# Performance work log

Measured on AMD Instinct MI355X. Metric: run time of the kernel, lower is better.

Reference implementation:

```python
import jax, jax.numpy as jnp
import numpy as np

B, S, F_IN, H, F_OUT, BB = 128, 1024, 128, 256, 128, 256


def setup_inputs() -> dict:
    key = jax.random.key(0)
    ks = jax.random.split(key, 16)
    s_in = 1.0 / np.sqrt(F_IN + H)
    s_bb = 1.0 / np.sqrt(BB)
    s_h = 1.0 / np.sqrt(H)
    return {
        "x": jax.random.normal(ks[0], (B, S, F_IN), dtype=jnp.float32),
        "ts": jax.random.uniform(ks[1], (B, S), dtype=jnp.float32),
        # backbone (depth=1): Linear(F_IN+H -> BB)
        "Wb": jax.random.normal(ks[2], (F_IN + H, BB), dtype=jnp.float32) * s_in,
        "bb": jnp.zeros((BB,), jnp.float32),
        # CfC heads: ff1, ff2, time_a, time_b (BB -> H)
        "Wff1": jax.random.normal(ks[3], (BB, H), dtype=jnp.float32) * s_bb,
        "bff1": jnp.zeros((H,), jnp.float32),
        "Wff2": jax.random.normal(ks[4], (BB, H), dtype=jnp.float32) * s_bb,
        "bff2": jnp.zeros((H,), jnp.float32),
        "Wta": jax.random.normal(ks[5], (BB, H), dtype=jnp.float32) * s_bb,
        "bta": jnp.zeros((H,), jnp.float32),
        "Wtb": jax.random.normal(ks[6], (BB, H), dtype=jnp.float32) * s_bb,
        "btb": jnp.zeros((H,), jnp.float32),
        # output projection Linear(H -> F_OUT)
        "Wout": jax.random.normal(ks[7], (H, F_OUT), dtype=jnp.float32) * s_h,
        "bout": jnp.zeros((F_OUT,), jnp.float32),
    }


def reference(x, ts, Wb, bb, Wff1, bff1, Wff2, bff2, Wta, bta, Wtb, btb, Wout, bout):
    # x: [B,S,F_IN], ts: [B,S] -> out: [B,S,F_OUT]
    batch = x.shape[0]
    hidden = Wff1.shape[1]

    def step(h, inp):
        xt, tt = inp  # xt: [B,F_IN], tt: [B]
        z = jnp.tanh(jnp.concatenate([xt, h], axis=-1) @ Wb + bb)  # backbone [B,BB]
        ff1 = jnp.tanh(z @ Wff1 + bff1)
        ff2 = jnp.tanh(z @ Wff2 + bff2)
        t_a = z @ Wta + bta
        t_b = z @ Wtb + btb
        t_interp = jax.nn.sigmoid(t_a * tt[:, None] + t_b)  # time-dependent gate
        h_new = ff1 * (1.0 - t_interp) + t_interp * ff2
        y = h_new @ Wout + bout
        return h_new, y

    h0 = jnp.zeros((batch, hidden), dtype=x.dtype)
    xs = (jnp.swapaxes(x, 0, 1), jnp.swapaxes(ts, 0, 1))  # time-major for scan
    _, ys = jax.lax.scan(step, h0, xs)  # ys: [S,B,F_OUT]
    return jnp.swapaxes(ys, 0, 1)
```

## Files before the change

kernel.cpp:

```cpp
#include <hip/hip_runtime.h>

#define Bn   128
#define Sn   1024
#define FIN  128
#define Hn   256
#define FOUT 128
#define KBB  384
#define NT1  512

#define NR4 20
#define NL4 1
#define DYN_SMEM ((32 * 256 * 8 + NL4 * 1024 * 8) * 2)

#define WB_OFF 0
#define W4_OFF 98304
#define WO_OFF 360448
#define WS_HALVES 393216
#define HBUF_OFF WS_HALVES
#define XC_OFF (HBUF_OFF + (size_t)Bn * Sn * Hn)
#define WS_SPLIT_BYTES ((size_t)(WS_HALVES + (size_t)Bn * Sn * Hn) * 2)
#define WS_FULL_BYTES ((XC_OFF + (size_t)Bn * Sn * Hn) * 2)

typedef _Float16 h2 __attribute__((ext_vector_type(2)));
typedef _Float16 h8 __attribute__((ext_vector_type(8)));

__device__ __forceinline__ float dot2f(h2 a, h2 b, float c) {
#if __has_builtin(__builtin_amdgcn_fdot2)
  return __builtin_amdgcn_fdot2(a, b, c, false);
#else
  return c + (float)a[0] * (float)b[0] + (float)a[1] * (float)b[1];
#endif
}
__device__ __forceinline__ void dot8_4(h8 v, h8 w, float& c0, float& c1, float& c2, float& c3) {
  h2 v0 = {v[0], v[1]}, v1 = {v[2], v[3]}, v2 = {v[4], v[5]}, v3 = {v[6], v[7]};
  h2 w0 = {w[0], w[1]}, w1 = {w[2], w[3]}, w2 = {w[4], w[5]}, w3 = {w[6], w[7]};
  c0 = dot2f(v0, w0, c0); c1 = dot2f(v1, w1, c1);
  c2 = dot2f(v2, w2, c2); c3 = dot2f(v3, w3, c3);
}

__global__ __launch_bounds__(256) void pack_w(
    const float* __restrict__ Wb, const float* __restrict__ W1,
    const float* __restrict__ W2, const float* __restrict__ W3,
    const float* __restrict__ W4, const float* __restrict__ Wo,
    _Float16* __restrict__ ws) {
  int p = blockIdx.x * 256 + threadIdx.x;
  if (p >= WS_HALVES) return;
  float v;
  if (p < W4_OFF) {
    int r = p & 7, j = (p >> 3) & 255;
    int k = ((p >> 11) << 3) | r;
    v = Wb[k * 256 + j];
  } else if (p < WO_OFF) {
    int q = p - W4_OFF;
    int r = q & 7, j = (q >> 3) & 1023;
    int k = ((q >> 13) << 3) | r;
    int jj = j & 255;
    const float* Ws = (j < 256) ? W1 : (j < 512) ? W2 : (j < 768) ? W3 : W4;
    v = Ws[k * 256 + jj];
  } else {
    int q = p - WO_OFF;
    int r = q & 7, j = (q >> 3) & 127;
    int k = ((q >> 10) << 3) | r;
    v = Wo[k * 128 + j];
  }
  ws[p] = (_Float16)v;
}

__global__ __launch_bounds__(256) void xgemm(
    const float* __restrict__ x, const _Float16* __restrict__ ws,
    _Float16* __restrict__ xc) {
  __shared__ __align__(16) _Float16 sX[64 * 128];
  const int tid = threadIdx.x;
  const size_t r0 = (size_t)blockIdx.x * 64;
  const float* xb = x + r0 * 128;
#pragma unroll
  for (int m = 0; m < 32; ++m)
    sX[m * 256 + tid] = (_Float16)xb[m * 256 + tid];
  const _Float16* gX = ws + WB_OFF + (size_t)tid * 8;
  h8 wx[16];
#pragma unroll
  for (int L = 0; L < 16; ++L) wx[L] = *(const h8*)(gX + (size_t)L * 2048);
  __syncthreads();
  for (int r = 0; r < 64; ++r) {
    float c0 = 0.f, c1 = 0.f, c2 = 0.f, c3 = 0.f;
#pragma unroll
    for (int L = 0; L < 16; ++L) {
      h8 v = *(const h8*)&sX[r * 128 + L * 8];
      dot8_4(v, wx[L], c0, c1, c2, c3);
    }
    xc[(r0 + r) * 256 + tid] = (_Float16)(c0 + c1 + c2 + c3);
  }
}

template <int XC, int INLINE_Y>
__global__ __launch_bounds__(NT1, 2) void cfc5(
    const float* __restrict__ x, const float* __restrict__ ts,
    const float* __restrict__ bb, const float* __restrict__ bf1,
    const float* __restrict__ bf2, const float* __restrict__ bta,
    const float* __restrict__ btb, const float* __restrict__ bo,
    _Float16* __restrict__ ws, float* __restrict__ out) {
  __shared__ __align__(16) _Float16 xh[KBB];
  __shared__ __align__(16) _Float16 zf[Hn];
  __shared__ float tsb[Sn];
  __shared__ float scrZ[256];
  __shared__ float scrH[512];
  extern __shared__ __align__(16) _Float16 dyn[];
  _Float16* sWb  = dyn;
  _Float16* sW4L = dyn + 32 * 256 * 8;

  const int tid = threadIdx.x;
  const int b = blockIdx.x;
  const _Float16* Wb_p = ws + WB_OFF;
  const _Float16* W4_p = ws + W4_OFF;
  const _Float16* Wo_p = ws + WO_OFF;
  _Float16* hbuf = ws + HBUF_OFF;
  const _Float16* xcp = ws + XC_OFF;

  const float* xrow  = x  + (size_t)b * Sn * FIN;
  const float* tsrow = ts + (size_t)b * Sn;
  float*       orow  = out + (size_t)b * Sn * FOUT;

  const int jz = tid & 255, kz = tid >> 8;
  const float bbj = (tid < 256) ? bb[tid] : 0.f;
  const float bHA = (tid < 256) ? bf1[tid] : bf2[tid - 256];
  const float bHB = (tid < 256) ? bta[tid] : btb[tid - 256];
  const int jY = tid & 127, kqY = tid >> 7;
  const float boj = bo[jY];

  if (XC) {
    const h8* src = (const h8*)(Wb_p + (size_t)16 * 2048);
    h8* dst = (h8*)sWb;
    for (int i = tid; i < 8192; i += NT1) dst[i] = src[i];
  }
  {
    const h8* src = (const h8*)(W4_p + (size_t)NR4 * 8192);
    h8* dst = (h8*)sW4L;
    for (int i = tid; i < NL4 * 1024; i += NT1) dst[i] = src[i];
  }
  for (int i = tid; i < Sn; i += NT1) tsb[i] = tsrow[i];
  if (tid < 128) ((unsigned*)xh)[64 + tid] = 0;
  if (!XC && tid < 64) {
    float2 xv = *(const float2*)(xrow + 2 * tid);
    h2 p; p[0] = (_Float16)xv.x; p[1] = (_Float16)xv.y;
    *(h2*)&xh[2 * tid] = p;
  }

  const _Float16* gA = W4_p + (size_t)tid * 8;
  const _Float16* gB = W4_p + (size_t)(tid + 512) * 8;
  h8 wA[NR4], wBv[NR4];
#pragma unroll
  for (int c = 0; c < NR4; ++c) {
    wA[c]  = *(const h8*)(gA + (size_t)c * 8192);
    wBv[c] = *(const h8*)(gB + (size_t)c * 8192);
  }
#pragma unroll
  for (int c = 0; c < NR4; ++c) {
    asm volatile("" : "+v"(wA[c]));
    asm volatile("" : "+v"(wBv[c]));
  }
  __syncthreads();

  for (int st = 0; st < Sn; ++st) {
    float xcv = 0.f;
    if (XC && tid < 256)
      xcv = (float)xcp[((size_t)b * Sn + st) * 256 + tid];
    float2 xv; xv.x = 0.f; xv.y = 0.f;
    if (!XC && tid >= 448 && st + 1 < Sn)
      xv = *(const float2*)(xrow + (size_t)(st + 1) * FIN + 2 * (tid - 448));

    float a0 = 0.f, a1 = 0.f, a2 = 0.f, a3 = 0.f;
    if (XC) {
#pragma unroll 4
      for (int c = 0; c < 16; ++c) {
        int kc = kz * 16 + c;
        h8 v = *(const h8*)&xh[128 + kc * 8];
        h8 w = *(const h8*)&sWb[((size_t)kc * 256 + jz) * 8];
        dot8_4(v, w, a0, a1, a2, a3);
      }
    } else {
      const _Float16* gZ = Wb_p + ((size_t)(kz * 24) * 256 + jz) * 8;
#pragma unroll 4
      for (int c = 0; c < 24; ++c) {
        h8 v = *(const h8*)&xh[(kz * 24 + c) * 8];
        h8 w = *(const h8*)(gZ + (size_t)c * 2048);
        dot8_4(v, w, a0, a1, a2, a3);
      }
    }
    float zs = a0 + a1 + a2 + a3;
    if (kz) scrZ[jz] = zs;
    __syncthreads();
    if (tid < 256) {
      float zp = zs + scrZ[tid] + bbj;
      if (XC) zp += xcv;
      zf[tid] = (_Float16)tanhf(zp);
    }
    if (!XC && tid >= 448 && st + 1 < Sn) {
      h2 p; p[0] = (_Float16)xv.x; p[1] = (_Float16)xv.y;
      *(h2*)&xh[2 * (tid - 448)] = p;
    }
    __syncthreads();

    float hA0 = 0.f, hA1 = 0.f, hA2 = 0.f, hA3 = 0.f;
    float hB0 = 0.f, hB1 = 0.f, hB2 = 0.f, hB3 = 0.f;
#pragma unroll 2
    for (int c = NR4 + NL4; c < 32; ++c) {
      h8 v  = *(const h8*)&zf[c * 8];
      h8 wa = *(const h8*)(gA + (size_t)c * 8192);
      h8 wb = *(const h8*)(gB + (size_t)c * 8192);
      dot8_4(v, wa, hA0, hA1, hA2, hA3);
      dot8_4(v, wb, hB0, hB1, hB2, hB3);
    }
#pragma unroll
    for (int c = 0; c < NR4; ++c) {
      h8 v = *(const h8*)&zf[c * 8];
      dot8_4(v, wA[c],  hA0, hA1, hA2, hA3);
      dot8_4(v, wBv[c], hB0, hB1, hB2, hB3);
    }
#pragma unroll
    for (int l = 0; l < NL4; ++l) {
      h8 v  = *(const h8*)&zf[(NR4 + l) * 8];
      h8 wa = *(const h8*)&sW4L[((size_t)l * 1024 + tid) * 8];
      h8 wb = *(const h8*)&sW4L[((size_t)l * 1024 + tid + 512) * 8];
      dot8_4(v, wa, hA0, hA1, hA2, hA3);
      dot8_4(v, wb, hB0, hB1, hB2, hB3);
    }
    float gAv = hA0 + hA1 + hA2 + hA3 + bHA;
    float gBv = hB0 + hB1 + hB2 + hB3 + bHB;
    if (tid >= 256) {
      scrH[tid - 256]       = gAv;
      scrH[256 + tid - 256] = gBv;
    }
    __syncthreads();
    if (tid < 256) {
      float ff2v = scrH[tid], tbv = scrH[256 + tid];
      float tt = tsb[st];
      float sg = 1.f / (1.f + __expf(-(gBv * tt + tbv)));
      float hn = tanhf(gAv) * (1.f - sg) + sg * tanhf(ff2v);
      xh[128 + tid] = (_Float16)hn;
      if (!INLINE_Y)
        hbuf[((size_t)b * Sn + st) * Hn + tid] = (_Float16)hn;
    }
    __syncthreads();

    if (INLINE_Y) {
      const _Float16* gY = Wo_p + ((size_t)(kqY * 8) * 128 + jY) * 8;
      float y0 = 0.f, y1 = 0.f, y2 = 0.f, y3 = 0.f;
#pragma unroll
      for (int c = 0; c < 8; ++c) {
        h8 v = *(const h8*)&xh[128 + (kqY * 8 + c) * 8];
        h8 w = *(const h8*)(gY + (size_t)c * 1024);
        dot8_4(v, w, y0, y1, y2, y3);
      }
      float ysv = y0 + y1 + y2 + y3;
      if (kqY) scrH[(kqY - 1) * 128 + jY] = ysv;
      __syncthreads();
      if (kqY == 0) {
        float y = ysv + boj + scrH[jY] + scrH[128 + jY] + scrH[256 + jY];
        orow[(size_t)st * FOUT + jY] = y;
      }
    }
  }
}

#define SMEMY (65536 + 4096)
extern "C" __global__ __launch_bounds__(256, 4)
void ygemm(const _Float16* __restrict__ ws, const float* __restrict__ bo,
           float* __restrict__ out) {
  extern __shared__ char ysm[];
  _Float16* sWo = (_Float16*)ysm;
  _Float16* sH  = (_Float16*)(ysm + 65536);
  const int tid = threadIdx.x;
  { const uint4* g = (const uint4*)(ws + WO_OFF);
    uint4* l = (uint4*)sWo;
#pragma unroll
    for (int i = 0; i < 16; ++i) l[tid + 256 * i] = g[tid + 256 * i]; }
  const _Float16* hb = ws + HBUF_OFF;
  const int row0 = blockIdx.x * 256;
  const int j = tid & 127, rh = tid >> 7;
  const float boj = bo[j];
  for (int it = 0; it < 32; ++it) {
    const int rbase = row0 + it * 8;
    __syncthreads();
    ((uint4*)sH)[tid] = ((const uint4*)(hb + (size_t)rbase * 256))[tid];
    __syncthreads();
#pragma unroll
    for (int rr = rh; rr < 8; rr += 2) {
      float y0 = 0.f, y1 = 0.f, y2 = 0.f, y3 = 0.f;
#pragma unroll 4
      for (int c = 0; c < 32; ++c) {
        h8 v = *(const h8*)&sH[rr * 256 + c * 8];
        h8 w = *(const h8*)&sWo[((size_t)c * 128 + j) * 8];
        dot8_4(v, w, y0, y1, y2, y3);
      }
      out[(size_t)(rbase + rr) * 128 + j] = y0 + y1 + y2 + y3 + boj;
    }
  }
}

extern "C" void kernel_launch(void* const* d_in, const int* in_sizes, int n_in,
                              void* d_out, int out_size, void* d_ws, size_t ws_size,
                              hipStream_t stream) {
  const float* x   = (const float*)d_in[0];
  const float* ts  = (const float*)d_in[1];
  const float* Wb  = (const float*)d_in[2];
  const float* bb  = (const float*)d_in[3];
  const float* W1  = (const float*)d_in[4];
  const float* bf1 = (const float*)d_in[5];
  const float* W2  = (const float*)d_in[6];
  const float* bf2 = (const float*)d_in[7];
  const float* W3  = (const float*)d_in[8];
  const float* bta = (const float*)d_in[9];
  const float* W4  = (const float*)d_in[10];
  const float* btb = (const float*)d_in[11];
  const float* Wo  = (const float*)d_in[12];
  const float* bo  = (const float*)d_in[13];
  float* out = (float*)d_out;
  _Float16* ws = (_Float16*)d_ws;

  pack_w<<<WS_HALVES / 256, 256, 0, stream>>>(Wb, W1, W2, W3, W4, Wo, ws);

  if (ws_size >= WS_FULL_BYTES) {
    xgemm<<<(Bn * Sn) / 64, 256, 0, stream>>>(x, ws, ws + XC_OFF);
    hipFuncSetAttribute((const void*)(cfc5<1, 0>),
                        hipFuncAttributeMaxDynamicSharedMemorySize, DYN_SMEM);
    cfc5<1, 0><<<Bn, NT1, DYN_SMEM, stream>>>(x, ts, bb, bf1, bf2, bta, btb, bo, ws, out);
    hipFuncSetAttribute((const void*)ygemm,
                        hipFuncAttributeMaxDynamicSharedMemorySize, SMEMY);
    ygemm<<<(Bn * Sn) / 256, 256, SMEMY, stream>>>(ws, bo, out);
  } else if (ws_size >= WS_SPLIT_BYTES) {
    hipFuncSetAttribute((const void*)(cfc5<0, 0>),
                        hipFuncAttributeMaxDynamicSharedMemorySize, DYN_SMEM);
    cfc5<0, 0><<<Bn, NT1, DYN_SMEM, stream>>>(x, ts, bb, bf1, bf2, bta, btb, bo, ws, out);
    hipFuncSetAttribute((const void*)ygemm,
                        hipFuncAttributeMaxDynamicSharedMemorySize, SMEMY);
    ygemm<<<(Bn * Sn) / 256, 256, SMEMY, stream>>>(ws, bo, out);
  } else {
    hipFuncSetAttribute((const void*)(cfc5<0, 1>),
                        hipFuncAttributeMaxDynamicSharedMemorySize, DYN_SMEM);
    cfc5<0, 1><<<Bn, NT1, DYN_SMEM, stream>>>(x, ts, bb, bf1, bf2, bta, btb, bo, ws, out);
  }
}
```

Before: 4.162 ms.

## Split each recurrent batch row across two blocks with global mailbox exchange

Adds a kernel, cfc6, that assigns each batch row to two workgroups, each owning half of the hidden units, so the launch covers 256 blocks instead of 128. At every timestep each block computes a partial backbone pre-activation from its own half of h and posts it to a double-buffered global mailbox. It then bumps a per-block counter and spin-waits on the partner's counter before adding the partner's partial. The aim is to halve the per-block weight work in the serial time loop and keep more of each block's head weights resident in LDS and registers. The cost is a global-memory handshake on every step, and the scheme relies on both blocks of a pair being co-resident, or it can deadlock.

```diff
diff --git a/kernel.cpp b/kernel.cpp
--- a/kernel.cpp
+++ b/kernel.cpp
@@ -11,6 +11,10 @@
 #define NR4 20
 #define NL4 1
 #define DYN_SMEM ((32 * 256 * 8 + NL4 * 1024 * 8) * 2)
+
+#define NL6 11
+#define PF6 10
+#define DYN6 ((16 * 256 * 8 + NL6 * 512 * 8) * 2)
 
 #define WB_OFF 0
 #define W4_OFF 98304
@@ -20,6 +24,10 @@
 #define XC_OFF (HBUF_OFF + (size_t)Bn * Sn * Hn)
 #define WS_SPLIT_BYTES ((size_t)(WS_HALVES + (size_t)Bn * Sn * Hn) * 2)
 #define WS_FULL_BYTES ((XC_OFF + (size_t)Bn * Sn * Hn) * 2)
+#define MBOX_BYTE_OFF WS_FULL_BYTES
+#define MBOX_FLOATS ((size_t)Bn * 2 * 2 * 256)
+#define CNT_BYTE_OFF (MBOX_BYTE_OFF + MBOX_FLOATS * 4)
+#define WS_PAIR_BYTES (CNT_BYTE_OFF + 256 * 4)
 
 typedef _Float16 h2 __attribute__((ext_vector_type(2)));
 typedef _Float16 h8 __attribute__((ext_vector_type(8)));
@@ -66,6 +74,8 @@
   ws[p] = (_Float16)v;
 }
 
+__global__ void zcnt(unsigned* __restrict__ c) { c[threadIdx.x] = 0; }
+
 __global__ __launch_bounds__(256) void xgemm(
     const float* __restrict__ x, const _Float16* __restrict__ ws,
     _Float16* __restrict__ xc) {
@@ -89,6 +99,128 @@
       dot8_4(v, wx[L], c0, c1, c2, c3);
     }
     xc[(r0 + r) * 256 + tid] = (_Float16)(c0 + c1 + c2 + c3);
+  }
+}
+
+__global__ __launch_bounds__(NT1) void cfc6(
+    const float* __restrict__ ts, const float* __restrict__ bb,
+    const float* __restrict__ bf1, const float* __restrict__ bf2,
+    const float* __restrict__ bta, const float* __restrict__ btb,
+    _Float16* __restrict__ ws, unsigned* __restrict__ cnt,
+    float* __restrict__ mbox) {
+  __shared__ __align__(16) _Float16 hl[128];
+  __shared__ __align__(16) _Float16 zfs[Hn];
+  __shared__ float tsb[Sn];
+  __shared__ float scrZ[256];
+  __shared__ float scrH[384];
+  extern __shared__ __align__(16) _Float16 dyn[];
+  _Float16* sWbh = dyn;
+  _Float16* sW4L = dyn + 16 * 256 * 8;
+
+  const int tid = threadIdx.x;
+  const int row = blockIdx.x & 127;
+  const int hf  = blockIdx.x >> 7;
+
+  const _Float16* Wb_p = ws + WB_OFF;
+  const _Float16* W4_p = ws + W4_OFF;
+  _Float16* hbuf = ws + HBUF_OFF;
+  const _Float16* xcp = ws + XC_OFF;
+  const float* tsrow = ts + (size_t)row * Sn;
+
+  const int jz = tid & 255, kq = tid >> 8;
+  const int head = tid >> 7, jj = tid & 127;
+  const int jcol = head * 256 + hf * 128 + jj;
+  const float bbj = (tid < 256) ? bb[tid] : 0.f;
+  const float bH =
+      (head == 0 ? bf1 : head == 1 ? bf2 : head == 2 ? bta : btb)[hf * 128 + jj];
+  const _Float16* gH = W4_p + (size_t)jcol * 8;
+
+  {
+    const h8* src = (const h8*)(Wb_p + (size_t)(16 + hf * 16) * 2048);
+    h8* dst = (h8*)sWbh;
+    for (int i = tid; i < 16 * 256; i += NT1) dst[i] = src[i];
+  }
+#pragma unroll
+  for (int c = 0; c < NL6; ++c)
+    *(h8*)&sW4L[((size_t)c * 512 + tid) * 8] = *(const h8*)(gH + (size_t)c * 8192);
+  for (int i = tid; i < Sn; i += NT1) tsb[i] = tsrow[i];
+  if (tid < 128) hl[tid] = (_Float16)0.f;
+
+  float* mb_me       = mbox + (size_t)(row * 2 + hf) * 512;
+  const float* mb_pt = mbox + (size_t)(row * 2 + (1 - hf)) * 512;
+  unsigned* c_me = cnt + row * 2 + hf;
+  unsigned* c_pt = cnt + row * 2 + (1 - hf);
+  __syncthreads();
+
+  for (unsigned st = 0; st < Sn; ++st) {
+    h8 wpf[PF6];
+#pragma unroll
+    for (int c = 0; c < PF6; ++c)
+      wpf[c] = *(const h8*)(gH + (size_t)(NL6 + c) * 8192);
+    float xcv = 0.f;
+    if (tid < 256) xcv = (float)xcp[((size_t)row * Sn + st) * 256 + tid];
+
+    float a0 = 0.f, a1 = 0.f, a2 = 0.f, a3 = 0.f;
+#pragma unroll
+    for (int c = kq * 8; c < kq * 8 + 8; ++c) {
+      h8 v = *(const h8*)&hl[c * 8];
+      h8 w = *(const h8*)&sWbh[((size_t)c * 256 + jz) * 8];
+      dot8_4(v, w, a0, a1, a2, a3);
+    }
+    float zs = a0 + a1 + a2 + a3;
+    if (kq) scrZ[jz] = zs;
+    __syncthreads();
+    float zp = 0.f;
+    if (tid < 256) {
+      zp = zs + scrZ[tid];
+      __hip_atomic_store(&mb_me[(st & 1) * 256 + tid], zp,
+                         __ATOMIC_RELAXED, __HIP_MEMORY_SCOPE_AGENT);
+    }
+    __syncthreads();
+    if (tid == 0) {
+      __hip_atomic_fetch_add(c_me, 1u, __ATOMIC_RELEASE, __HIP_MEMORY_SCOPE_AGENT);
+      while (__hip_atomic_load(c_pt, __ATOMIC_ACQUIRE, __HIP_MEMORY_SCOPE_AGENT) <= st)
+        __builtin_amdgcn_s_sleep(1);
+    }
+    __syncthreads();
+    if (tid < 256) {
+      float pz = __hip_atomic_load(&mb_pt[(st & 1) * 256 + tid],
+                                   __ATOMIC_RELAXED, __HIP_MEMORY_SCOPE_AGENT);
+      zfs[tid] = (_Float16)tanhf(zp + pz + xcv + bbj);
+    }
+    __syncthreads();
+
+    float s0 = 0.f, s1 = 0.f, s2 = 0.f, s3 = 0.f;
+#pragma unroll 2
+    for (int c = NL6 + PF6; c < 32; ++c) {
+      h8 v = *(const h8*)&zfs[c * 8];
+      h8 w = *(const h8*)(gH + (size_t)c * 8192);
+      dot8_4(v, w, s0, s1, s2, s3);
+    }
+#pragma unroll
+    for (int c = 0; c < PF6; ++c) {
+      h8 v = *(const h8*)&zfs[(NL6 + c) * 8];
+      dot8_4(v, wpf[c], s0, s1, s2, s3);
+    }
+    float b0 = 0.f, b1 = 0.f, b2 = 0.f, b3 = 0.f;
+#pragma unroll
+    for (int c = 0; c < NL6; ++c) {
+      h8 v = *(const h8*)&zfs[c * 8];
+      h8 w = *(const h8*)&sW4L[((size_t)c * 512 + tid) * 8];
+      dot8_4(v, w, b0, b1, b2, b3);
+    }
+    float g = (s0 + b0) + (s1 + b1) + (s2 + b2) + (s3 + b3) + bH;
+    if (head) scrH[(head - 1) * 128 + jj] = g;
+    __syncthreads();
+    if (head == 0) {
+      float ff2 = scrH[jj], ta = scrH[128 + jj], tb = scrH[256 + jj];
+      float tt = tsb[st];
+      float sg = 1.f / (1.f + __expf(-(ta * tt + tb)));
+      float hn = tanhf(g) * (1.f - sg) + sg * tanhf(ff2);
+      hl[jj] = (_Float16)hn;
+      hbuf[((size_t)row * Sn + st) * Hn + hf * 128 + jj] = (_Float16)hn;
+    }
+    __syncthreads();
   }
 }
 
@@ -319,7 +451,19 @@
 
   pack_w<<<WS_HALVES / 256, 256, 0, stream>>>(Wb, W1, W2, W3, W4, Wo, ws);
 
-  if (ws_size >= WS_FULL_BYTES) {
+  if (ws_size >= WS_PAIR_BYTES) {
+    zcnt<<<1, 256, 0, stream>>>((unsigned*)((char*)d_ws + CNT_BYTE_OFF));
+    xgemm<<<(Bn * Sn) / 64, 256, 0, stream>>>(x, ws, ws + XC_OFF);
+    hipFuncSetAttribute((const void*)cfc6,
+                        hipFuncAttributeMaxDynamicSharedMemorySize, DYN6);
+    cfc6<<<2 * Bn, NT1, DYN6, stream>>>(
+        ts, bb, bf1, bf2, bta, btb, ws,
+        (unsigned*)((char*)d_ws + CNT_BYTE_OFF),
+        (float*)((char*)d_ws + MBOX_BYTE_OFF));
+    hipFuncSetAttribute((const void*)ygemm,
+                        hipFuncAttributeMaxDynamicSharedMemorySize, SMEMY);
+    ygemm<<<(Bn * Sn) / 256, 256, SMEMY, stream>>>(ws, bo, out);
+  } else if (ws_size >= WS_FULL_BYTES) {
     xgemm<<<(Bn * Sn) / 64, 256, 0, stream>>>(x, ws, ws + XC_OFF);
     hipFuncSetAttribute((const void*)(cfc5<1, 0>),
                         hipFuncAttributeMaxDynamicSharedMemorySize, DYN_SMEM);
```

Result: slower. 11.16 ms (+168.0%).
